# Optimization experiments

Measured on AMD Instinct MI355X. Metric: run time of the kernel, lower is better.

The kernel has to match this reference:

```python
import jax, jax.numpy as jnp
import numpy as np

V, K, M_FWD, M_BWD = 100000, 64, 16, 16
SIGMA = 1.0

def _alpha_init(key, m_half, k):
    # banded init: -10 everywhere, 0 on a strided band, + 0.1*randn
    a = np.full((m_half, k), -10.0, dtype=np.float32)
    stride = max(1, k // m_half)
    for i in range(m_half):
        a[i, i * stride: min(i * stride + stride, k)] = 0.0
    return jnp.asarray(a) + 0.1 * jax.random.normal(key, (m_half, k), dtype=jnp.float32)

def setup_inputs() -> dict:
    key = jax.random.key(0)
    k1, k2, k3, k4 = jax.random.split(key, 4)
    return {
        "d_out_t": jax.random.normal(k1, (V, K), dtype=jnp.float32),
        "d_in_t": jax.random.normal(k2, (V, K), dtype=jnp.float32),
        "alpha_fwd": _alpha_init(k3, M_FWD, K),
        "alpha_bwd": _alpha_init(k4, M_BWD, K),
    }

def _compress(phi, alpha, sigma):
    # phi: (V, K); alpha: (m_half, K) -> z: (V, m_half, K)
    z = phi[:, None, :] + alpha[None, :, :]
    return sigma * jax.scipy.special.logsumexp(z / sigma, axis=-1)

def reference(d_out_t, d_in_t, alpha_fwd, alpha_bwd):
    y_fwd = _compress(d_out_t, alpha_fwd, SIGMA)  # (V, m_fwd)
    y_bwd = _compress(d_in_t, alpha_bwd, SIGMA)   # (V, m_bwd)
    return (y_fwd, y_bwd)
```

## Files before the change

### kernel.cpp

```cpp
#include <hip/hip_runtime.h>


#define K_DIM 64

__global__ __launch_bounds__(256) void dual_compress_kernel(
    const float* __restrict__ d_out_t,
    const float* __restrict__ d_in_t,
    const float* __restrict__ alpha_fwd,
    const float* __restrict__ alpha_bwd,
    float* __restrict__ out, int V)
{
    __shared__ float ealpha[32 * K_DIM];

    int tid = threadIdx.x;
    #pragma unroll
    for (int it = 0; it < 8; ++it) {
        int i = tid + it * 256;
        float a = (i < 1024) ? alpha_fwd[i] : alpha_bwd[i - 1024];
        ealpha[i] = __expf(a);
    }
    __syncthreads();

    int lane = tid & 63;
    int w    = tid >> 6;
    int c    = w & 1;
    int rh   = w >> 1;
    int v    = blockIdx.x * 128 + rh * 64 + lane;
    if (v >= V) return;

    const float* phi = (c == 0 ? d_out_t : d_in_t) + (size_t)v * K_DIM;

    float4 e4[16];
    #pragma unroll
    for (int i = 0; i < 16; ++i) {
        float4 p = ((const float4*)phi)[i];
        e4[i].x = __expf(p.x);
        e4[i].y = __expf(p.y);
        e4[i].z = __expf(p.z);
        e4[i].w = __expf(p.w);
    }

    const float4* arow_base = (const float4*)&ealpha[c * 16 * K_DIM];

    float y[16];
    #pragma unroll
    for (int mi = 0; mi < 16; ++mi) {
        const float4* a4 = arow_base + mi * 16;
        float acc = 0.0f;
        #pragma unroll
        for (int k = 0; k < 16; ++k) {
            float4 a = a4[k];
            acc = fmaf(e4[k].x, a.x, acc);
            acc = fmaf(e4[k].y, a.y, acc);
            acc = fmaf(e4[k].z, a.z, acc);
            acc = fmaf(e4[k].w, a.w, acc);
        }
        y[mi] = __logf(acc);
    }

    float* orow = out + ((size_t)c * V + v) * 16;
    #pragma unroll
    for (int i = 0; i < 4; ++i)
        ((float4*)orow)[i] = make_float4(y[4*i], y[4*i+1], y[4*i+2], y[4*i+3]);
}

extern "C" void kernel_launch(void* const* d_in, const int* in_sizes, int n_in,
                              void* d_out, int out_size, void* d_ws, size_t ws_size,
                              hipStream_t stream) {
    const float* d_out_t   = (const float*)d_in[0];
    const float* d_in_t    = (const float*)d_in[1];
    const float* alpha_fwd = (const float*)d_in[2];
    const float* alpha_bwd = (const float*)d_in[3];
    float* out = (float*)d_out;

    int V = in_sizes[0] / K_DIM;
    int grid = (V + 127) / 128;

    dual_compress_kernel<<<grid, 256, 0, stream>>>(
        d_out_t, d_in_t, alpha_fwd, alpha_bwd, out, V);
}
```

Measured before the change: 100.9 us.

## Precompute exp(alpha) in a prep kernel and read it via scalar loads

Moves the exp(alpha) table from per-block shared memory into a workspace buffer filled by a small prep kernel. The main kernel then reads it through wave-uniform addresses (readfirstlane), so the compiler can use scalar loads instead of LDS reads, and the block-level sync goes away. The loop order becomes k-outer with 16 accumulators, and out-of-range rows are clamped instead of returning early. The trade-offs are an extra kernel launch and reliance on scalar-cache hits for the 8KB table.

```diff
diff --git a/kernel.cpp b/kernel.cpp
--- a/kernel.cpp
+++ b/kernel.cpp
@@ -3,65 +3,72 @@
 
 #define K_DIM 64
 
+__global__ __launch_bounds__(256) void prep_ealpha_kernel(
+    const float* __restrict__ alpha_fwd,
+    const float* __restrict__ alpha_bwd,
+    float* __restrict__ ea)
+{
+    int i = blockIdx.x * 256 + threadIdx.x;
+    float a = (i < 1024) ? alpha_fwd[i] : alpha_bwd[i - 1024];
+    ea[i] = __expf(a);
+}
+
 __global__ __launch_bounds__(256) void dual_compress_kernel(
     const float* __restrict__ d_out_t,
     const float* __restrict__ d_in_t,
-    const float* __restrict__ alpha_fwd,
-    const float* __restrict__ alpha_bwd,
+    const float* __restrict__ ea,
     float* __restrict__ out, int V)
 {
-    __shared__ float ealpha[32 * K_DIM];
-
-    int tid = threadIdx.x;
-    #pragma unroll
-    for (int it = 0; it < 8; ++it) {
-        int i = tid + it * 256;
-        float a = (i < 1024) ? alpha_fwd[i] : alpha_bwd[i - 1024];
-        ealpha[i] = __expf(a);
-    }
-    __syncthreads();
-
+    int tid  = threadIdx.x;
     int lane = tid & 63;
     int w    = tid >> 6;
     int c    = w & 1;
     int rh   = w >> 1;
     int v    = blockIdx.x * 128 + rh * 64 + lane;
-    if (v >= V) return;
+    int vc   = (v < V) ? v : (V - 1);
 
-    const float* phi = (c == 0 ? d_out_t : d_in_t) + (size_t)v * K_DIM;
+    const float* base = c ? d_in_t : d_out_t;
+    const float4* p = (const float4*)(base + (size_t)vc * K_DIM);
 
     float4 e4[16];
     #pragma unroll
     for (int i = 0; i < 16; ++i) {
-        float4 p = ((const float4*)phi)[i];
-        e4[i].x = __expf(p.x);
-        e4[i].y = __expf(p.y);
-        e4[i].z = __expf(p.z);
-        e4[i].w = __expf(p.w);
+        float4 q = p[i];
+        e4[i].x = __expf(q.x); e4[i].y = __expf(q.y);
+        e4[i].z = __expf(q.z); e4[i].w = __expf(q.w);
     }
 
-    const float4* arow_base = (const float4*)&ealpha[c * 16 * K_DIM];
+    const float* eac = ea + __builtin_amdgcn_readfirstlane(c << 10);
 
-    float y[16];
+    float acc[16];
     #pragma unroll
-    for (int mi = 0; mi < 16; ++mi) {
-        const float4* a4 = arow_base + mi * 16;
-        float acc = 0.0f;
+    for (int mi = 0; mi < 16; ++mi) acc[mi] = 0.0f;
+
+    #pragma unroll
+    for (int kc = 0; kc < 16; ++kc) {
+        float4 e = e4[kc];
         #pragma unroll
-        for (int k = 0; k < 16; ++k) {
-            float4 a = a4[k];
-            acc = fmaf(e4[k].x, a.x, acc);
-            acc = fmaf(e4[k].y, a.y, acc);
-            acc = fmaf(e4[k].z, a.z, acc);
-            acc = fmaf(e4[k].w, a.w, acc);
+        for (int mi = 0; mi < 16; ++mi) {
+            const float* arow = eac + mi * K_DIM + kc * 4;
+            acc[mi] = fmaf(e.x, arow[0], acc[mi]);
+            acc[mi] = fmaf(e.y, arow[1], acc[mi]);
+            acc[mi] = fmaf(e.z, arow[2], acc[mi]);
+            acc[mi] = fmaf(e.w, arow[3], acc[mi]);
         }
-        y[mi] = __logf(acc);
     }
 
-    float* orow = out + ((size_t)c * V + v) * 16;
-    #pragma unroll
-    for (int i = 0; i < 4; ++i)
-        ((float4*)orow)[i] = make_float4(y[4*i], y[4*i+1], y[4*i+2], y[4*i+3]);
+    if (v < V) {
+        float* orow = out + ((size_t)c * V + v) * 16;
+        #pragma unroll
+        for (int i = 0; i < 4; ++i) {
+            float4 y;
+            y.x = __logf(acc[4*i+0]);
+            y.y = __logf(acc[4*i+1]);
+            y.z = __logf(acc[4*i+2]);
+            y.w = __logf(acc[4*i+3]);
+            ((float4*)orow)[i] = y;
+        }
+    }
 }
 
 extern "C" void kernel_launch(void* const* d_in, const int* in_sizes, int n_in,
@@ -72,10 +79,13 @@
     const float* alpha_fwd = (const float*)d_in[2];
     const float* alpha_bwd = (const float*)d_in[3];
     float* out = (float*)d_out;
+    float* ea  = (float*)d_ws;
 
     int V = in_sizes[0] / K_DIM;
+
+    prep_ealpha_kernel<<<8, 256, 0, stream>>>(alpha_fwd, alpha_bwd, ea);
+
     int grid = (V + 127) / 128;
-
     dual_compress_kernel<<<grid, 256, 0, stream>>>(
-        d_out_t, d_in_t, alpha_fwd, alpha_bwd, out, V);
+        d_out_t, d_in_t, ea, out, V);
 }
```

After: 101.5 us. No clear change (+0.7%).
